# Performance work log

Measured on AMD Instinct MI355X. Metric: run time of the kernel, lower is better.

Reference implementation:

```python
import jax, jax.numpy as jnp
import numpy as np

DIM = 768
NUM_HEADS = 12
HEAD_DIM = DIM // NUM_HEADS
SCALE = HEAD_DIM ** -0.5


def setup_inputs() -> dict:
    key = jax.random.key(0)
    k1, k2, k3, k4 = jax.random.split(key, 4)
    x = jax.random.normal(k1, (8, 1024, DIM), dtype=jnp.float32)
    # torch Linear weights are [out, in]; no qkv bias (qkv_bias=False)
    qkv_w = jax.random.normal(k2, (3 * DIM, DIM), dtype=jnp.float32) * (DIM ** -0.5)
    proj_w = jax.random.normal(k3, (DIM, DIM), dtype=jnp.float32) * (DIM ** -0.5)
    proj_b = jax.random.normal(k4, (DIM,), dtype=jnp.float32) * 0.02
    return {"x": x, "qkv_w": qkv_w, "proj_w": proj_w, "proj_b": proj_b}


def reference(x, qkv_w, proj_w, proj_b):
    B, N, C = x.shape
    # qkv: [B, N, 3C] -> [3, B, H, N, D]
    qkv = jnp.einsum('bnc,oc->bno', x, qkv_w)
    qkv = qkv.reshape(B, N, 3, NUM_HEADS, HEAD_DIM).transpose(2, 0, 3, 1, 4)
    q, k, v = qkv[0], qkv[1], qkv[2]
    attn = jnp.einsum('bhnd,bhmd->bhnm', q, k) * SCALE
    attn = jax.nn.softmax(attn, axis=-1)
    out = jnp.einsum('bhnm,bhmd->bhnd', attn, v)  # [B, H, N, D]
    out = out.transpose(0, 2, 1, 3).reshape(B, N, C)
    out = jnp.einsum('bnc,oc->bno', out, proj_w) + proj_b
    return out
```

## Files before the change

kernel.cpp:

```cpp
#include <hip/hip_runtime.h>

typedef short bf16x8 __attribute__((ext_vector_type(8)));
typedef float f32x4 __attribute__((ext_vector_type(4)));

#define AS1 __attribute__((address_space(1)))
#define AS3 __attribute__((address_space(3)))

__device__ __forceinline__ void gload16(const void* g, void* l) {
  __builtin_amdgcn_global_load_lds((const AS1 void*)g, (AS3 void*)l, 16, 0, 0);
}

__device__ __forceinline__ unsigned short f2bf(float f) {
  union { float f; unsigned u; } v; v.f = f;
  unsigned r = v.u + 0x7FFFu + ((v.u >> 16) & 1u);
  return (unsigned short)(r >> 16);
}

__device__ __forceinline__ unsigned cvtpk(float a, float b) {
  unsigned r;
  asm("v_cvt_pk_bf16_f32 %0, %1, %2" : "=v"(r) : "v"(a), "v"(b));
  return r;
}


__global__ __launch_bounds__(256) void cast_kernel(const float* __restrict__ in,
                                                   unsigned short* __restrict__ out, int n4) {
  int i = blockIdx.x * blockDim.x + threadIdx.x;
  if (i < n4) {
    float4 v = reinterpret_cast<const float4*>(in)[i];
    ushort4 o; o.x = f2bf(v.x); o.y = f2bf(v.y); o.z = f2bf(v.z); o.w = f2bf(v.w);
    reinterpret_cast<ushort4*>(out)[i] = o;
  }
}

template<int MODE>
__global__ __launch_bounds__(256) void gemm128(
    const unsigned short* __restrict__ A, const unsigned short* __restrict__ B,
    int K, int N,
    unsigned short* __restrict__ Qh, unsigned short* __restrict__ Kh,
    unsigned short* __restrict__ Vt,
    float* __restrict__ Cf, const float* __restrict__ bias) {
  constexpr int BM = (MODE == 0) ? 128 : 64;
  constexpr int MREP = BM / 32;
  __shared__ unsigned short Ab[BM * 64];
  __shared__ unsigned short Bb[128 * 64];
  const int tid = threadIdx.x, lane = tid & 63, wave = tid >> 6;
  const int l15 = lane & 15, lhi = lane >> 4;
  const int m0 = blockIdx.y * BM, n0 = blockIdx.x * 128;
  const int wr = wave >> 1, wc = wave & 1;

  f32x4 acc[MREP][4] = {};

  const int srow = tid >> 3;
  const int scol = (((tid & 7) * 16) ^ ((srow & 7) << 4)) >> 1;
  const unsigned short* aSrc = A + (size_t)(m0 + srow) * K + scol;
  const unsigned short* bSrc = B + (size_t)(n0 + srow) * K + scol;
  char* ldsA = (char*)Ab + wave * 1024;
  char* ldsB = (char*)Bb + wave * 1024;

  const int rswz = (l15 & 7) << 4;

  for (int k0 = 0; k0 < K; k0 += 64) {
    __syncthreads();
#pragma unroll
    for (int i = 0; i < BM / 32; ++i)
      gload16(aSrc + k0 + (size_t)32 * K * i, ldsA + i * 4096);
#pragma unroll
    for (int i = 0; i < 4; ++i)
      gload16(bSrc + k0 + (size_t)32 * K * i, ldsB + i * 4096);
    __syncthreads();
#pragma unroll
    for (int ks = 0; ks < 2; ++ks) {
      bf16x8 af[MREP], bfr[4];
#pragma unroll
      for (int mm = 0; mm < MREP; ++mm)
        af[mm] = *reinterpret_cast<const bf16x8*>(
            (char*)Ab + (wr * (BM / 2) + mm * 16 + l15) * 128 + ((ks * 64 + lhi * 16) ^ rswz));
#pragma unroll
      for (int nn = 0; nn < 4; ++nn)
        bfr[nn] = *reinterpret_cast<const bf16x8*>(
            (char*)Bb + (wc * 64 + nn * 16 + l15) * 128 + ((ks * 64 + lhi * 16) ^ rswz));
#pragma unroll
      for (int mm = 0; mm < MREP; ++mm)
#pragma unroll
        for (int nn = 0; nn < 4; ++nn)
          acc[mm][nn] = __builtin_amdgcn_mfma_f32_16x16x32_bf16(af[mm], bfr[nn], acc[mm][nn], 0, 0, 0);
    }
  }

  if (MODE == 0) {
    const int region = (n0 >= 1536) ? 2 : (n0 >= 768 ? 1 : 0);
#pragma unroll
    for (int mm = 0; mm < MREP; ++mm) {
      int gm = m0 + wr * (BM / 2) + mm * 16 + lhi * 4;
      int bb = gm >> 10, nb = gm & 1023;
#pragma unroll
      for (int nn = 0; nn < 4; ++nn) {
        int gn = n0 + wc * 64 + nn * 16 + l15 - region * 768;
        int d = gn & 63, hh = gn >> 6;
        if (region == 2) {
          ushort4 o;
          o.x = f2bf(acc[mm][nn][0]); o.y = f2bf(acc[mm][nn][1]);
          o.z = f2bf(acc[mm][nn][2]); o.w = f2bf(acc[mm][nn][3]);
          *reinterpret_cast<ushort4*>(&Vt[((size_t)(bb * 12 + hh) * 64 + d) * 1024 + nb]) = o;
        } else {
          unsigned short* dst =
              (region == 0 ? Qh : Kh) + ((size_t)(bb * 12 + hh) * 1024 + nb) * 64 + d;
#pragma unroll
          for (int r = 0; r < 4; ++r) dst[(size_t)r * 64] = f2bf(acc[mm][nn][r]);
        }
      }
    }
  } else {
#pragma unroll
    for (int mm = 0; mm < MREP; ++mm) {
      int gm = m0 + wr * (BM / 2) + mm * 16 + lhi * 4;
#pragma unroll
      for (int nn = 0; nn < 4; ++nn) {
        int gn = n0 + wc * 64 + nn * 16 + l15;
        float bv = bias[gn];
#pragma unroll
        for (int r = 0; r < 4; ++r)
          Cf[(size_t)(gm + r) * N + gn] = acc[mm][nn][r] + bv;
      }
    }
  }
}

__global__ __launch_bounds__(256) void attn_kernel(
    const unsigned short* __restrict__ qh, const unsigned short* __restrict__ kh,
    const unsigned short* __restrict__ vt, unsigned short* __restrict__ aout) {
  __shared__ unsigned short KT[2][4096];
  __shared__ unsigned short VT[2][4096];
  __shared__ unsigned short P[4][2048];
  __shared__ float Al[4][32];
  __shared__ float Li[4][32];

  const int tid = threadIdx.x, lane = tid & 63, wave = tid >> 6;
  const int l15 = lane & 15, lhi = lane >> 4;
  const int bh = blockIdx.x % 96, qt = blockIdx.x / 96;
  const int b = bh / 12, h = bh % 12;
  const float c1 = 0.125f * 1.44269504088896340736f;

  const int srow = tid >> 3;
  const int scol = (((tid & 7) * 16) ^ ((srow & 7) << 4)) >> 1;
  const unsigned short* kS0 = kh + ((size_t)bh * 1024 + srow) * 64 + scol;
  const unsigned short* kS1 = kS0 + (size_t)32 * 64;
  const unsigned short* vS0 = vt + ((size_t)bh * 64 + srow) * 1024 + scol;
  const unsigned short* vS1 = vS0 + (size_t)32 * 1024;
  char* kD = (char*)&KT[0][0] + wave * 1024;
  char* vD = (char*)&VT[0][0] + wave * 1024;

  const int qw0 = qt * 128 + wave * 32;
  bf16x8 qf[2][2];
#pragma unroll
  for (int rb = 0; rb < 2; ++rb)
#pragma unroll
    for (int ks = 0; ks < 2; ++ks)
      qf[rb][ks] = *reinterpret_cast<const bf16x8*>(
          qh + ((size_t)bh * 1024 + qw0 + rb * 16 + l15) * 64 + ks * 32 + lhi * 8);

  f32x4 oacc[2][4] = {};
  float mrun[2] = {-1e30f, -1e30f};
  float lsum[2] = {0.f, 0.f};

  const int rswz = (l15 & 7) << 4;
  const int fo0 = l15 * 128 + ((lhi * 16) ^ rswz);
  const int fo1 = l15 * 128 + ((64 + lhi * 16) ^ rswz);
  unsigned short* pl = &P[wave][0];

  gload16(kS0, kD); gload16(kS1, kD + 4096);
  gload16(vS0, vD); gload16(vS1, vD + 4096);

  for (int kt = 0; kt < 16; ++kt) {
    const int cur = kt & 1;
    if (kt < 15) {
      const int kv = (kt + 1) * 64;
      char* kd = kD + (cur ^ 1) * 8192;
      char* vd = vD + (cur ^ 1) * 8192;
      gload16(kS0 + (size_t)kv * 64, kd); gload16(kS1 + (size_t)kv * 64, kd + 4096);
      gload16(vS0 + kv, vd); gload16(vS1 + kv, vd + 4096);
      asm volatile("s_waitcnt vmcnt(4)" ::: "memory");
    } else {
      asm volatile("s_waitcnt vmcnt(0)" ::: "memory");
    }
    __builtin_amdgcn_s_barrier();

    const char* kb = (const char*)&KT[cur][0];
    const char* vb = (const char*)&VT[cur][0];

    f32x4 s[2][4] = {};
#pragma unroll
    for (int nt = 0; nt < 4; ++nt) {
      bf16x8 kf0 = *reinterpret_cast<const bf16x8*>(kb + nt * 2048 + fo0);
      bf16x8 kf1 = *reinterpret_cast<const bf16x8*>(kb + nt * 2048 + fo1);
#pragma unroll
      for (int rb = 0; rb < 2; ++rb) {
        s[rb][nt] = __builtin_amdgcn_mfma_f32_16x16x32_bf16(kf0, qf[rb][0], s[rb][nt], 0, 0, 0);
        s[rb][nt] = __builtin_amdgcn_mfma_f32_16x16x32_bf16(kf1, qf[rb][1], s[rb][nt], 0, 0, 0);
      }
    }

    float mt[2];
#pragma unroll
    for (int rb = 0; rb < 2; ++rb) {
      float a0 = fmaxf(fmaxf(s[rb][0][0], s[rb][0][1]), fmaxf(s[rb][0][2], s[rb][0][3]));
      float a1 = fmaxf(fmaxf(s[rb][1][0], s[rb][1][1]), fmaxf(s[rb][1][2], s[rb][1][3]));
      float a2 = fmaxf(fmaxf(s[rb][2][0], s[rb][2][1]), fmaxf(s[rb][2][2], s[rb][2][3]));
      float a3 = fmaxf(fmaxf(s[rb][3][0], s[rb][3][1]), fmaxf(s[rb][3][2], s[rb][3][3]));
      float rm = fmaxf(fmaxf(a0, a1), fmaxf(a2, a3));
      rm = fmaxf(rm, __shfl_xor(rm, 16, 64));
      rm = fmaxf(rm, __shfl_xor(rm, 32, 64));
      mt[rb] = rm * c1;
    }

    bool ok = (mt[0] - mrun[0] <= 8.f) && (mt[1] - mrun[1] <= 8.f);
    if (!__all(ok)) {
      float al[2];
#pragma unroll
      for (int rb = 0; rb < 2; ++rb) {
        float mn = fmaxf(mrun[rb], mt[rb]);
        al[rb] = __builtin_amdgcn_exp2f(mrun[rb] - mn);
        mrun[rb] = mn;
        lsum[rb] *= al[rb];
      }
      if (lhi == 0) { Al[wave][l15] = al[0]; Al[wave][16 + l15] = al[1]; }
#pragma unroll
      for (int rb = 0; rb < 2; ++rb) {
        f32x4 av = *reinterpret_cast<const f32x4*>(&Al[wave][rb * 16 + lhi * 4]);
#pragma unroll
        for (int dt = 0; dt < 4; ++dt)
#pragma unroll
          for (int r = 0; r < 4; ++r) oacc[rb][dt][r] *= av[r];
      }
    }

#pragma unroll
    for (int rb = 0; rb < 2; ++rb) {
#pragma unroll
      for (int nt = 0; nt < 4; ++nt)
#pragma unroll
        for (int r = 0; r < 4; ++r)
          s[rb][nt][r] = __builtin_amdgcn_exp2f(__builtin_fmaf(s[rb][nt][r], c1, -mrun[rb]));

      float b0 = (s[rb][0][0] + s[rb][0][1]) + (s[rb][0][2] + s[rb][0][3]);
      float b1 = (s[rb][1][0] + s[rb][1][1]) + (s[rb][1][2] + s[rb][1][3]);
      float b2 = (s[rb][2][0] + s[rb][2][1]) + (s[rb][2][2] + s[rb][2][3]);
      float b3 = (s[rb][3][0] + s[rb][3][1]) + (s[rb][3][2] + s[rb][3][3]);
      lsum[rb] += (b0 + b1) + (b2 + b3);
    }

#pragma unroll
    for (int rb = 0; rb < 2; ++rb)
#pragma unroll
      for (int nt = 0; nt < 4; ++nt) {
        uint2 wv;
        wv.x = cvtpk(s[rb][nt][0], s[rb][nt][1]);
        wv.y = cvtpk(s[rb][nt][2], s[rb][nt][3]);
        *reinterpret_cast<uint2*>(
            (char*)pl + rb * 2048 + l15 * 128 + ((nt * 32 + lhi * 8) ^ rswz)) = wv;
      }

    bf16x8 paf[2][2];
#pragma unroll
    for (int rb = 0; rb < 2; ++rb) {
      paf[rb][0] = *reinterpret_cast<const bf16x8*>((char*)pl + rb * 2048 + fo0);
      paf[rb][1] = *reinterpret_cast<const bf16x8*>((char*)pl + rb * 2048 + fo1);
    }

#pragma unroll
    for (int dt = 0; dt < 4; ++dt) {
      bf16x8 vf0 = *reinterpret_cast<const bf16x8*>(vb + dt * 2048 + fo0);
      bf16x8 vf1 = *reinterpret_cast<const bf16x8*>(vb + dt * 2048 + fo1);
#pragma unroll
      for (int rb = 0; rb < 2; ++rb) {
        oacc[rb][dt] = __builtin_amdgcn_mfma_f32_16x16x32_bf16(paf[rb][0], vf0, oacc[rb][dt], 0, 0, 0);
        oacc[rb][dt] = __builtin_amdgcn_mfma_f32_16x16x32_bf16(paf[rb][1], vf1, oacc[rb][dt], 0, 0, 0);
      }
    }
    __builtin_amdgcn_s_barrier();
  }

  float ls[2];
#pragma unroll
  for (int rb = 0; rb < 2; ++rb) {
    float v = lsum[rb];
    v += __shfl_xor(v, 16, 64);
    v += __shfl_xor(v, 32, 64);
    ls[rb] = v;
  }
  if (lhi == 0) { Li[wave][l15] = ls[0]; Li[wave][16 + l15] = ls[1]; }
#pragma unroll
  for (int rb = 0; rb < 2; ++rb) {
    f32x4 lv = *reinterpret_cast<const f32x4*>(&Li[wave][rb * 16 + lhi * 4]);
    float inv[4];
#pragma unroll
    for (int r = 0; r < 4; ++r) inv[r] = 1.f / lv[r];
#pragma unroll
    for (int dt = 0; dt < 4; ++dt)
#pragma unroll
      for (int r = 0; r < 4; ++r) {
        int n = qw0 + rb * 16 + lhi * 4 + r;
        int d = dt * 16 + l15;
        aout[((size_t)(b * 1024 + n)) * 768 + h * 64 + d] = f2bf(oacc[rb][dt][r] * inv[r]);
      }
  }
}

extern "C" void kernel_launch(void* const* d_in, const int* in_sizes, int n_in,
                              void* d_out, int out_size, void* d_ws, size_t ws_size,
                              hipStream_t stream) {
  const float* x      = (const float*)d_in[0];
  const float* qkv_w  = (const float*)d_in[1];
  const float* proj_w = (const float*)d_in[2];
  const float* proj_b = (const float*)d_in[3];
  float* out = (float*)d_out;

  char* ws = (char*)d_ws;
  unsigned short* xb     = (unsigned short*)(ws);
  unsigned short* wqkvb  = (unsigned short*)(ws + 12582912);
  unsigned short* wprojb = (unsigned short*)(ws + 16121856);
  unsigned short* qhb    = (unsigned short*)(ws + 17301504);
  unsigned short* khb    = (unsigned short*)(ws + 29884416);
  unsigned short* vtb    = (unsigned short*)(ws + 42467328);
  unsigned short* aob    = (unsigned short*)(ws + 55050240);

  cast_kernel<<<6144, 256, 0, stream>>>(x, xb, 1572864);
  cast_kernel<<<1728, 256, 0, stream>>>(qkv_w, wqkvb, 442368);
  cast_kernel<<<576, 256, 0, stream>>>(proj_w, wprojb, 147456);

  dim3 g1(2304 / 128, 8192 / 128);
  gemm128<0><<<g1, 256, 0, stream>>>(xb, wqkvb, 768, 2304, qhb, khb, vtb, nullptr, nullptr);

  attn_kernel<<<96 * 8, 256, 0, stream>>>(qhb, khb, vtb, aob);

  dim3 g2(768 / 128, 8192 / 64);
  gemm128<1><<<g2, 256, 0, stream>>>(aob, wprojb, 768, 768, nullptr, nullptr, nullptr, out, proj_b);
}
```

Baseline: 129.0 us.

## Switch attention to 32x32 MFMA with register-resident P via permlane swap

Rewrites the attention inner loop to use 32x32x16 bf16 MFMAs with transposed score layout, so each lane owns one query row. The probability fragments are converted in registers using v_permlane32_swap instead of a round trip through LDS, and the shared-memory buffers for P, alpha and row sums go away. It also fuses the three cast launches into one kernel and adds s_setprio around the MFMA blocks. The K/V prefetch now waits on all loads at the top of each iteration, which may cut overlap between loads and compute.

After: 125.8 us. -2.5%, faster.

```diff
diff --git a/kernel.cpp b/kernel.cpp
--- a/kernel.cpp
+++ b/kernel.cpp
@@ -2,6 +2,7 @@
 
 typedef short bf16x8 __attribute__((ext_vector_type(8)));
 typedef float f32x4 __attribute__((ext_vector_type(4)));
+typedef float f32x16 __attribute__((ext_vector_type(16)));
 
 #define AS1 __attribute__((address_space(1)))
 #define AS3 __attribute__((address_space(3)))
@@ -21,16 +22,22 @@
   asm("v_cvt_pk_bf16_f32 %0, %1, %2" : "=v"(r) : "v"(a), "v"(b));
   return r;
 }
-
-
-__global__ __launch_bounds__(256) void cast_kernel(const float* __restrict__ in,
-                                                   unsigned short* __restrict__ out, int n4) {
+__device__ __forceinline__ void plswap(unsigned& d, unsigned& s) {
+  asm("v_permlane32_swap_b32 %0, %1" : "+v"(d), "+v"(s));
+}
+
+__global__ __launch_bounds__(256) void cast_all(
+    const float* __restrict__ x, const float* __restrict__ w1, const float* __restrict__ w2,
+    unsigned short* __restrict__ xb, unsigned short* __restrict__ w1b,
+    unsigned short* __restrict__ w2b) {
   int i = blockIdx.x * blockDim.x + threadIdx.x;
-  if (i < n4) {
-    float4 v = reinterpret_cast<const float4*>(in)[i];
-    ushort4 o; o.x = f2bf(v.x); o.y = f2bf(v.y); o.z = f2bf(v.z); o.w = f2bf(v.w);
-    reinterpret_cast<ushort4*>(out)[i] = o;
-  }
+  const float* in; unsigned short* out;
+  if (i < 1572864) { in = x; out = xb; }
+  else if (i < 2015232) { i -= 1572864; in = w1; out = w1b; }
+  else { i -= 2015232; in = w2; out = w2b; }
+  float4 v = reinterpret_cast<const float4*>(in)[i];
+  ushort4 o; o.x = f2bf(v.x); o.y = f2bf(v.y); o.z = f2bf(v.z); o.w = f2bf(v.w);
+  reinterpret_cast<ushort4*>(out)[i] = o;
 }
 
 template<int MODE>
@@ -132,12 +139,9 @@
     const unsigned short* __restrict__ vt, unsigned short* __restrict__ aout) {
   __shared__ unsigned short KT[2][4096];
   __shared__ unsigned short VT[2][4096];
-  __shared__ unsigned short P[4][2048];
-  __shared__ float Al[4][32];
-  __shared__ float Li[4][32];
 
   const int tid = threadIdx.x, lane = tid & 63, wave = tid >> 6;
-  const int l15 = lane & 15, lhi = lane >> 4;
+  const int l31 = lane & 31, hi = lane >> 5;
   const int bh = blockIdx.x % 96, qt = blockIdx.x / 96;
   const int b = bh / 12, h = bh % 12;
   const float c1 = 0.125f * 1.44269504088896340736f;
@@ -152,159 +156,124 @@
   char* vD = (char*)&VT[0][0] + wave * 1024;
 
   const int qw0 = qt * 128 + wave * 32;
-  bf16x8 qf[2][2];
-#pragma unroll
-  for (int rb = 0; rb < 2; ++rb)
-#pragma unroll
-    for (int ks = 0; ks < 2; ++ks)
-      qf[rb][ks] = *reinterpret_cast<const bf16x8*>(
-          qh + ((size_t)bh * 1024 + qw0 + rb * 16 + l15) * 64 + ks * 32 + lhi * 8);
-
-  f32x4 oacc[2][4] = {};
-  float mrun[2] = {-1e30f, -1e30f};
-  float lsum[2] = {0.f, 0.f};
-
-  const int rswz = (l15 & 7) << 4;
-  const int fo0 = l15 * 128 + ((lhi * 16) ^ rswz);
-  const int fo1 = l15 * 128 + ((64 + lhi * 16) ^ rswz);
-  unsigned short* pl = &P[wave][0];
+  const unsigned short* qbase = qh + ((size_t)bh * 1024 + qw0 + l31) * 64 + hi * 8;
+  bf16x8 qf[4];
+#pragma unroll
+  for (int ks = 0; ks < 4; ++ks)
+    qf[ks] = *reinterpret_cast<const bf16x8*>(qbase + ks * 16);
+
+  f32x16 oacc[2] = {};
+  float mrun = -1e30f, lsum = 0.f;
+
+  const int swz = (l31 & 7) << 4;
+  const int rowb = l31 * 128;
+
+  auto mkfrag = [&](const f32x16& e, int s8) -> bf16x8 {
+    unsigned A0 = cvtpk(e[s8 + 0], e[s8 + 1]);
+    unsigned A1 = cvtpk(e[s8 + 2], e[s8 + 3]);
+    unsigned B0 = cvtpk(e[s8 + 4], e[s8 + 5]);
+    unsigned B1 = cvtpk(e[s8 + 6], e[s8 + 7]);
+    plswap(A0, B0);
+    plswap(A1, B1);
+    union { unsigned u[4]; bf16x8 v; } wu;
+    wu.u[0] = A0; wu.u[1] = A1; wu.u[2] = B0; wu.u[3] = B1;
+    return wu.v;
+  };
 
   gload16(kS0, kD); gload16(kS1, kD + 4096);
   gload16(vS0, vD); gload16(vS1, vD + 4096);
 
   for (int kt = 0; kt < 16; ++kt) {
     const int cur = kt & 1;
+    asm volatile("s_waitcnt vmcnt(0)" ::: "memory");
+    __builtin_amdgcn_s_barrier();
     if (kt < 15) {
       const int kv = (kt + 1) * 64;
       char* kd = kD + (cur ^ 1) * 8192;
       char* vd = vD + (cur ^ 1) * 8192;
       gload16(kS0 + (size_t)kv * 64, kd); gload16(kS1 + (size_t)kv * 64, kd + 4096);
       gload16(vS0 + kv, vd); gload16(vS1 + kv, vd + 4096);
-      asm volatile("s_waitcnt vmcnt(4)" ::: "memory");
-    } else {
-      asm volatile("s_waitcnt vmcnt(0)" ::: "memory");
-    }
-    __builtin_amdgcn_s_barrier();
+    }
 
     const char* kb = (const char*)&KT[cur][0];
     const char* vb = (const char*)&VT[cur][0];
 
-    f32x4 s[2][4] = {};
-#pragma unroll
-    for (int nt = 0; nt < 4; ++nt) {
-      bf16x8 kf0 = *reinterpret_cast<const bf16x8*>(kb + nt * 2048 + fo0);
-      bf16x8 kf1 = *reinterpret_cast<const bf16x8*>(kb + nt * 2048 + fo1);
-#pragma unroll
-      for (int rb = 0; rb < 2; ++rb) {
-        s[rb][nt] = __builtin_amdgcn_mfma_f32_16x16x32_bf16(kf0, qf[rb][0], s[rb][nt], 0, 0, 0);
-        s[rb][nt] = __builtin_amdgcn_mfma_f32_16x16x32_bf16(kf1, qf[rb][1], s[rb][nt], 0, 0, 0);
-      }
-    }
-
-    float mt[2];
-#pragma unroll
-    for (int rb = 0; rb < 2; ++rb) {
-      float a0 = fmaxf(fmaxf(s[rb][0][0], s[rb][0][1]), fmaxf(s[rb][0][2], s[rb][0][3]));
-      float a1 = fmaxf(fmaxf(s[rb][1][0], s[rb][1][1]), fmaxf(s[rb][1][2], s[rb][1][3]));
-      float a2 = fmaxf(fmaxf(s[rb][2][0], s[rb][2][1]), fmaxf(s[rb][2][2], s[rb][2][3]));
-      float a3 = fmaxf(fmaxf(s[rb][3][0], s[rb][3][1]), fmaxf(s[rb][3][2], s[rb][3][3]));
-      float rm = fmaxf(fmaxf(a0, a1), fmaxf(a2, a3));
-      rm = fmaxf(rm, __shfl_xor(rm, 16, 64));
-      rm = fmaxf(rm, __shfl_xor(rm, 32, 64));
-      mt[rb] = rm * c1;
-    }
-
-    bool ok = (mt[0] - mrun[0] <= 8.f) && (mt[1] - mrun[1] <= 8.f);
-    if (!__all(ok)) {
-      float al[2];
-#pragma unroll
-      for (int rb = 0; rb < 2; ++rb) {
-        float mn = fmaxf(mrun[rb], mt[rb]);
-        al[rb] = __builtin_amdgcn_exp2f(mrun[rb] - mn);
-        mrun[rb] = mn;
-        lsum[rb] *= al[rb];
-      }
-      if (lhi == 0) { Al[wave][l15] = al[0]; Al[wave][16 + l15] = al[1]; }
-#pragma unroll
-      for (int rb = 0; rb < 2; ++rb) {
-        f32x4 av = *reinterpret_cast<const f32x4*>(&Al[wave][rb * 16 + lhi * 4]);
-#pragma unroll
-        for (int dt = 0; dt < 4; ++dt)
-#pragma unroll
-          for (int r = 0; r < 4; ++r) oacc[rb][dt][r] *= av[r];
-      }
-    }
-
-#pragma unroll
-    for (int rb = 0; rb < 2; ++rb) {
-#pragma unroll
-      for (int nt = 0; nt < 4; ++nt)
-#pragma unroll
-        for (int r = 0; r < 4; ++r)
-          s[rb][nt][r] = __builtin_amdgcn_exp2f(__builtin_fmaf(s[rb][nt][r], c1, -mrun[rb]));
-
-      float b0 = (s[rb][0][0] + s[rb][0][1]) + (s[rb][0][2] + s[rb][0][3]);
-      float b1 = (s[rb][1][0] + s[rb][1][1]) + (s[rb][1][2] + s[rb][1][3]);
-      float b2 = (s[rb][2][0] + s[rb][2][1]) + (s[rb][2][2] + s[rb][2][3]);
-      float b3 = (s[rb][3][0] + s[rb][3][1]) + (s[rb][3][2] + s[rb][3][3]);
-      lsum[rb] += (b0 + b1) + (b2 + b3);
-    }
-
-#pragma unroll
-    for (int rb = 0; rb < 2; ++rb)
-#pragma unroll
-      for (int nt = 0; nt < 4; ++nt) {
-        uint2 wv;
-        wv.x = cvtpk(s[rb][nt][0], s[rb][nt][1]);
-        wv.y = cvtpk(s[rb][nt][2], s[rb][nt][3]);
-        *reinterpret_cast<uint2*>(
-            (char*)pl + rb * 2048 + l15 * 128 + ((nt * 32 + lhi * 8) ^ rswz)) = wv;
-      }
-
-    bf16x8 paf[2][2];
-#pragma unroll
-    for (int rb = 0; rb < 2; ++rb) {
-      paf[rb][0] = *reinterpret_cast<const bf16x8*>((char*)pl + rb * 2048 + fo0);
-      paf[rb][1] = *reinterpret_cast<const bf16x8*>((char*)pl + rb * 2048 + fo1);
-    }
-
-#pragma unroll
-    for (int dt = 0; dt < 4; ++dt) {
-      bf16x8 vf0 = *reinterpret_cast<const bf16x8*>(vb + dt * 2048 + fo0);
-      bf16x8 vf1 = *reinterpret_cast<const bf16x8*>(vb + dt * 2048 + fo1);
-#pragma unroll
-      for (int rb = 0; rb < 2; ++rb) {
-        oacc[rb][dt] = __builtin_amdgcn_mfma_f32_16x16x32_bf16(paf[rb][0], vf0, oacc[rb][dt], 0, 0, 0);
-        oacc[rb][dt] = __builtin_amdgcn_mfma_f32_16x16x32_bf16(paf[rb][1], vf1, oacc[rb][dt], 0, 0, 0);
-      }
-    }
-    __builtin_amdgcn_s_barrier();
+    f32x16 p0 = {}, p1 = {};
+    __builtin_amdgcn_s_setprio(1);
+#pragma unroll
+    for (int ks = 0; ks < 4; ++ks) {
+      bf16x8 k0 = *reinterpret_cast<const bf16x8*>(kb + rowb + ((ks * 32 + hi * 16) ^ swz));
+      bf16x8 k1 = *reinterpret_cast<const bf16x8*>(kb + 4096 + rowb + ((ks * 32 + hi * 16) ^ swz));
+      p0 = __builtin_amdgcn_mfma_f32_32x32x16_bf16(k0, qf[ks], p0, 0, 0, 0);
+      p1 = __builtin_amdgcn_mfma_f32_32x32x16_bf16(k1, qf[ks], p1, 0, 0, 0);
+    }
+    __builtin_amdgcn_s_setprio(0);
+
+    float t8[8];
+#pragma unroll
+    for (int i = 0; i < 8; ++i)
+      t8[i] = fmaxf(fmaxf(p0[i], p0[i + 8]), fmaxf(p1[i], p1[i + 8]));
+    float t4[4];
+#pragma unroll
+    for (int i = 0; i < 4; ++i) t4[i] = fmaxf(t8[i], t8[i + 4]);
+    float rm = fmaxf(fmaxf(t4[0], t4[1]), fmaxf(t4[2], t4[3]));
+    rm = fmaxf(rm, __shfl_xor(rm, 32, 64));
+    float mt = rm * c1;
+
+    if (!__all(mt - mrun <= 8.f)) {
+      float mn = fmaxf(mrun, mt);
+      float al = __builtin_amdgcn_exp2f(mrun - mn);
+      mrun = mn;
+      lsum *= al;
+#pragma unroll
+      for (int i = 0; i < 16; ++i) { oacc[0][i] *= al; oacc[1][i] *= al; }
+    }
+
+#pragma unroll
+    for (int i = 0; i < 16; ++i) {
+      p0[i] = __builtin_amdgcn_exp2f(__builtin_fmaf(p0[i], c1, -mrun));
+      p1[i] = __builtin_amdgcn_exp2f(__builtin_fmaf(p1[i], c1, -mrun));
+    }
+
+    float su[8];
+#pragma unroll
+    for (int i = 0; i < 8; ++i)
+      su[i] = (p0[i] + p0[i + 8]) + (p1[i] + p1[i + 8]);
+    float s4[4];
+#pragma unroll
+    for (int i = 0; i < 4; ++i) s4[i] = su[i] + su[i + 4];
+    lsum += (s4[0] + s4[1]) + (s4[2] + s4[3]);
+
+    bf16x8 pb[4];
+    pb[0] = mkfrag(p0, 0); pb[1] = mkfrag(p0, 8);
+    pb[2] = mkfrag(p1, 0); pb[3] = mkfrag(p1, 8);
+
+    __builtin_amdgcn_s_setprio(1);
+#pragma unroll
+    for (int kseg = 0; kseg < 4; ++kseg) {
+      bf16x8 v0 = *reinterpret_cast<const bf16x8*>(vb + rowb + ((kseg * 32 + hi * 16) ^ swz));
+      bf16x8 v1 = *reinterpret_cast<const bf16x8*>(vb + 4096 + rowb + ((kseg * 32 + hi * 16) ^ swz));
+      oacc[0] = __builtin_amdgcn_mfma_f32_32x32x16_bf16(v0, pb[kseg], oacc[0], 0, 0, 0);
+      oacc[1] = __builtin_amdgcn_mfma_f32_32x32x16_bf16(v1, pb[kseg], oacc[1], 0, 0, 0);
+    }
+    __builtin_amdgcn_s_setprio(0);
   }
 
-  float ls[2];
-#pragma unroll
-  for (int rb = 0; rb < 2; ++rb) {
-    float v = lsum[rb];
-    v += __shfl_xor(v, 16, 64);
-    v += __shfl_xor(v, 32, 64);
-    ls[rb] = v;
-  }
-  if (lhi == 0) { Li[wave][l15] = ls[0]; Li[wave][16 + l15] = ls[1]; }
-#pragma unroll
-  for (int rb = 0; rb < 2; ++rb) {
-    f32x4 lv = *reinterpret_cast<const f32x4*>(&Li[wave][rb * 16 + lhi * 4]);
-    float inv[4];
-#pragma unroll
-    for (int r = 0; r < 4; ++r) inv[r] = 1.f / lv[r];
-#pragma unroll
-    for (int dt = 0; dt < 4; ++dt)
-#pragma unroll
-      for (int r = 0; r < 4; ++r) {
-        int n = qw0 + rb * 16 + lhi * 4 + r;
-        int d = dt * 16 + l15;
-        aout[((size_t)(b * 1024 + n)) * 768 + h * 64 + d] = f2bf(oacc[rb][dt][r] * inv[r]);
-      }
-  }
+  lsum += __shfl_xor(lsum, 32, 64);
+  float inv = 1.f / lsum;
+#pragma unroll
+  for (int dblk = 0; dblk < 2; ++dblk)
+#pragma unroll
+    for (int g = 0; g < 4; ++g) {
+      ushort4 o;
+      o.x = f2bf(oacc[dblk][4 * g + 0] * inv);
+      o.y = f2bf(oacc[dblk][4 * g + 1] * inv);
+      o.z = f2bf(oacc[dblk][4 * g + 2] * inv);
+      o.w = f2bf(oacc[dblk][4 * g + 3] * inv);
+      int d = dblk * 32 + 8 * g + 4 * hi;
+      *reinterpret_cast<ushort4*>(
+          aout + ((size_t)(b * 1024 + qw0 + l31)) * 768 + h * 64 + d) = o;
+    }
 }
 
 extern "C" void kernel_launch(void* const* d_in, const int* in_sizes, int n_in,
@@ -325,9 +294,7 @@
   unsigned short* vtb    = (unsigned short*)(ws + 42467328);
   unsigned short* aob    = (unsigned short*)(ws + 55050240);
 
-  cast_kernel<<<6144, 256, 0, stream>>>(x, xb, 1572864);
-  cast_kernel<<<1728, 256, 0, stream>>>(qkv_w, wqkvb, 442368);
-  cast_kernel<<<576, 256, 0, stream>>>(proj_w, wprojb, 147456);
+  cast_all<<<8448, 256, 0, stream>>>(x, qkv_w, proj_w, xb, wqkvb, wprojb);
 
   dim3 g1(2304 / 128, 8192 / 128);
   gemm128<0><<<g1, 256, 0, stream>>>(xb, wqkvb, 768, 2304, qhb, khb, vtb, nullptr, nullptr);
```
